# Optimization experiments

Hardware: AMD Instinct MI355X
Metric: run time of the kernel (lower is better)

Reference implementation:

```python
import jax, jax.numpy as jnp
import numpy as np

BINS = 256
EPS = 1e-8


def _norm255(x):
    # (x - min) / (max - min) * 255, truncated to int (torch .int())
    mx = jnp.max(x, axis=(2, 3), keepdims=True)
    mn = jnp.min(x, axis=(2, 3), keepdims=True)
    return ((x - mn) / (mx - mn) * 255.0).astype(jnp.int32)


def _hist256(x):
    # x int32 [B,C,H,W] -> per-(b,c) 256-bin histogram [B,C,256] float32
    B, C = x.shape[0], x.shape[1]
    flat = x.reshape(B * C, -1)
    rows = jnp.arange(B * C)[:, None]
    h = jnp.zeros((B * C, BINS), jnp.float32).at[rows, flat].add(1.0)
    return h.reshape(B, C, BINS)


def _entropy(x):
    # faithful to Entropy(): p = hist / (H*W); h = -sum p*log(p+1e-8)
    B, C, H, W = x.shape
    p = _hist256(x) / (H * W)
    h = -jnp.sum(p * jnp.log(p + EPS), axis=2)
    return h[:, :, None, None]  # [B,C,1,1]


def _joint_entropy(x_p, x_ms):
    # Faithful to Joint_entropy's quirky count: for each (i,j) it counts pixels
    # where (x_ms==i AND x_p==j) OR (x_ms!=i AND x_p!=j).
    # count[i,j] = 2*J[i,j] + npix - hist_ms[i] - hist_p[j], J = joint histogram.
    B, C, H, W = x_ms.shape
    npix = H * W
    bins = jnp.arange(BINS)
    M = (x_ms.reshape(B, C, npix)[..., None] == bins).astype(jnp.float32)  # [B,C,P,256]
    P = (x_p.reshape(B, npix)[..., None] == bins).astype(jnp.float32)      # [B,P,256]
    J = jnp.einsum('bcpi,bpj->bcij', M, P)                                  # [B,C,256,256]
    hist_ms = jnp.sum(M, axis=2)  # [B,C,256]
    hist_p = jnp.sum(P, axis=1)   # [B,256]
    count = 2.0 * J + npix - hist_ms[:, :, :, None] - hist_p[:, None, None, :]
    p = count / float(BINS * BINS)  # original divides by 256*256, not npix
    h = -jnp.sum(p * jnp.log(p + EPS), axis=(2, 3))
    return h[:, :, None, None]  # [B,C,1,1]


def _channel(f_p, f_ms):
    B, C, H, W = f_p.shape
    f_p_m = jnp.mean(f_p, axis=1, keepdims=True)  # [B,1,H,W]
    # AdaptiveAvgPool2d((16,16)) with H,W divisible by 16 == block mean
    pooled = f_p.reshape(B, C, 16, H // 16, 16, W // 16).mean(axis=(3, 5))
    f_p_a = jnp.mean(pooled, axis=1, keepdims=True)  # [B,1,16,16]
    f_ms_n = _norm255(f_ms)
    f_p_m_n = _norm255(f_p_m)
    f_p_a_n = _norm255(f_p_a)
    h_ms = _entropy(f_ms_n)                 # [B,C,1,1]
    h_p = _entropy(f_p_m_n)                 # [B,1,1,1]
    h_ms_p = _joint_entropy(f_p_a_n, f_ms_n)  # [B,C,1,1]
    mi = h_p + h_ms - h_ms_p
    mi = jax.nn.softmax(mi, axis=1)  # nn.Softmax() on 4D -> dim=1
    return f_ms + f_ms * mi


def _similarity(f_p, f_ms):
    B, C, H, W = f_p.shape
    f_ms_u = jax.image.resize(f_ms, (B, C, H, W), method='bilinear')
    a = f_ms_u.reshape(B, C, -1)
    b = f_p.reshape(B, C, -1)
    a = a - jnp.mean(a, axis=2, keepdims=True)
    b = b - jnp.mean(b, axis=2, keepdims=True)
    na = jnp.sqrt(jnp.sum(a * a, axis=2))  # [B,C] (ms norms)
    nb = jnp.sqrt(jnp.sum(b * b, axis=2))  # [B,C] (p norms)
    s = jnp.einsum('bcp,bdp->bcd', a, b)   # [B,C,C]
    return s / ((na * nb) / 100.0)[:, :, None]


def _spatial(f_p, f_ms):
    B, C, H, W = f_p.shape
    s_m = _similarity(f_p, f_ms)
    mx = jnp.max(s_m, axis=2)        # [B,C]
    idx = jnp.argmax(s_m, axis=2)    # [B,C] best f_p channel per ms channel
    scores = jax.nn.softmax(mx, axis=1)
    brow = jnp.arange(B)[:, None]
    # group score: sum of softmax scores of ms-channels that picked value v
    g = jnp.zeros((B, C), scores.dtype).at[brow, idx].add(scores)
    cnt = jnp.zeros((B, C), jnp.int32).at[brow, idx].add(1)
    k = jnp.min(jnp.sum(cnt > 0, axis=1))  # min #unique over batch
    min_k = (k + 1) // 2                   # ceil(min_k / 2)
    order = jnp.argsort(-g, axis=1)        # descending group score; absent groups (0) sort last
    sorted_scores = jnp.take_along_axis(g, order, axis=1)  # [B,C]
    pos_mask = jnp.arange(C) < min_k       # keep top min_k positions
    z = jnp.where(pos_mask[None, :], sorted_scores, -jnp.inf)
    w = jax.nn.softmax(z, axis=1)          # softmax over selected scores, 0 elsewhere
    gathered = jnp.take_along_axis(f_p, order[:, :, None, None], axis=1)  # [B,C,H,W]
    mask = jnp.sum(w[:, :, None, None] * jax.nn.sigmoid(gathered), axis=1, keepdims=True)
    return f_p + f_p * mask


def setup_inputs() -> dict:
    key = jax.random.key(0)
    k1, k2 = jax.random.split(key)
    f_p = jax.random.normal(k1, (8, 64, 256, 256), dtype=jnp.float32)
    f_ms = jax.random.normal(k2, (8, 64, 16, 16), dtype=jnp.float32)
    return {"f_p": f_p, "f_ms": f_ms}


def reference(f_p, f_ms):
    rel_ms = _channel(f_p, f_ms)
    rel_p = _spatial(f_p, f_ms)
    return (rel_p, rel_ms)
```

## Files before the change

kernel.cpp:

```cpp
#include <hip/hip_runtime.h>

#define BB 8
#define CC 64
#define HP 256
#define WP 256
#define PP 65536
#define QQ 256

__device__ __forceinline__ unsigned encF(float f) {
    unsigned u = __float_as_uint(f);
    return (u & 0x80000000u) ? ~u : (u | 0x80000000u);
}
__device__ __forceinline__ float decF(unsigned u) {
    unsigned b = (u & 0x80000000u) ? (u ^ 0x80000000u) : ~u;
    return __uint_as_float(b);
}

__device__ __forceinline__ double blockSumD(double v, double* red4) {
    int t = threadIdx.x;
    for (int d = 32; d; d >>= 1) v += __shfl_down(v, d, 64);
    __syncthreads();
    if ((t & 63) == 0) red4[t >> 6] = v;
    __syncthreads();
    double r = red4[0] + red4[1] + red4[2] + red4[3];
    __syncthreads();
    return r;
}

__global__ __launch_bounds__(256) void k34_fused(const float* __restrict__ fp,
                                                 const float* __restrict__ fms,
                                                 double* __restrict__ pasumD,
                                                 float* __restrict__ gtent,
                                                 double* __restrict__ chsumD,
                                                 double* __restrict__ chsumsqD,
                                                 int* __restrict__ msn,
                                                 int* __restrict__ histms,
                                                 float* __restrict__ hmsE,
                                                 float* __restrict__ naArr,
                                                 float* __restrict__ mssum) {
    int blk = blockIdx.x;
    if (blk < 4096) {
        int qg = blk & 7, c = (blk >> 3) & 63, b = blk >> 9;
        int x = threadIdx.x, s = x >> 4, r = x & 15;
        const float* src = fp + (size_t)(b * CC + c) * PP;
        __shared__ float tentL[256];
        __shared__ double red4[4];
        tentL[x] = 0.0f;
        __syncthreads();
        float wm, w0, wp;
        if (x <= 7)        { wm = 0.f; w0 = 1.f; wp = 0.f; }
        else if (x >= 248) { wm = 0.f; w0 = 1.f; wp = 0.f; }
        else if (r < 8)    { float fx = ((float)r + 8.5f) * 0.0625f; wm = 1.f - fx; w0 = fx;       wp = 0.f; }
        else               { float fx = ((float)r - 7.5f) * 0.0625f; wm = 0.f;      w0 = 1.f - fx; wp = fx;  }
        double sum = 0.0, ssq = 0.0;
#pragma unroll
        for (int qi = 0; qi < 2; ++qi) {
            int q = qg * 2 + qi;
            float am = 0.f, a0 = 0.f, ap = 0.f, cs = 0.f;
#pragma unroll
            for (int ry = 0; ry < 16; ++ry) {
                float v = src[(q * 16 + ry) * 256 + x];
                sum += (double)v;
                ssq += (double)v * (double)v;
                cs  += v;
                if ((q == 0 && ry < 8) || (q == 15 && ry >= 8)) {
                    a0 += v;
                } else if (ry < 8) {
                    float fy = ((float)ry + 8.5f) * 0.0625f;
                    am += (1.f - fy) * v; a0 += fy * v;
                } else {
                    float fy = ((float)ry - 7.5f) * 0.0625f;
                    a0 += (1.f - fy) * v; ap += fy * v;
                }
            }
            float vals[10];
            vals[0] = am * wm; vals[1] = am * w0; vals[2] = am * wp;
            vals[3] = a0 * wm; vals[4] = a0 * w0; vals[5] = a0 * wp;
            vals[6] = ap * wm; vals[7] = ap * w0; vals[8] = ap * wp;
            vals[9] = cs;
#pragma unroll
            for (int d = 8; d; d >>= 1) {
#pragma unroll
                for (int k2 = 0; k2 < 10; ++k2) vals[k2] += __shfl_down(vals[k2], d, 16);
            }
            if (r == 0) {
                if (q > 0) {
                    if (s > 0)  atomicAdd(&tentL[(q - 1) * 16 + (s - 1)], vals[0]);
                    atomicAdd(&tentL[(q - 1) * 16 + s], vals[1]);
                    if (s < 15) atomicAdd(&tentL[(q - 1) * 16 + (s + 1)], vals[2]);
                }
                if (s > 0)  atomicAdd(&tentL[q * 16 + (s - 1)], vals[3]);
                atomicAdd(&tentL[q * 16 + s], vals[4]);
                if (s < 15) atomicAdd(&tentL[q * 16 + (s + 1)], vals[5]);
                if (q < 15) {
                    if (s > 0)  atomicAdd(&tentL[(q + 1) * 16 + (s - 1)], vals[6]);
                    atomicAdd(&tentL[(q + 1) * 16 + s], vals[7]);
                    if (s < 15) atomicAdd(&tentL[(q + 1) * 16 + (s + 1)], vals[8]);
                }
                atomicAdd(&pasumD[b * 256 + q * 16 + s], (double)vals[9]);
            }
        }
        __syncthreads();
        int row = x >> 4;
        int rlo = qg * 2 - 1; if (rlo < 0) rlo = 0;
        int rhi = qg * 2 + 2; if (rhi > 15) rhi = 15;
        if (row >= rlo && row <= rhi) {
            atomicAdd(&gtent[(size_t)(b * CC + c) * QQ + x], tentL[x]);
        }
        double st = blockSumD(sum, red4);
        double sq = blockSumD(ssq, red4);
        if (x == 0) {
            atomicAdd(&chsumD[b * CC + c], st);
            atomicAdd(&chsumsqD[b * CC + c], sq);
        }
    } else {
        int blk2 = blk - 4096, b = blk2 >> 6, c = blk2 & 63, t = threadIdx.x;
        __shared__ float m[256];
        __shared__ int hist[256];
        __shared__ double red4[4];
        __shared__ double U[256];
        __shared__ unsigned umn, umx;
        float v = fms[(size_t)(b * CC + c) * QQ + t];
        m[t] = v;
        hist[t] = 0;
        if (t == 0) { umn = 0xFFFFFFFFu; umx = 0u; }
        float mn = v, mx = v;
        for (int d = 32; d; d >>= 1) {
            mn = fminf(mn, __shfl_down(mn, d, 64));
            mx = fmaxf(mx, __shfl_down(mx, d, 64));
        }
        __syncthreads();
        if ((t & 63) == 0) { atomicMin(&umn, encF(mn)); atomicMax(&umx, encF(mx)); }
        __syncthreads();
        mn = decF(umn); mx = decF(umx);
        int bin = (int)((v - mn) / (mx - mn) * 255.0f);
        bin = min(max(bin, 0), 255);
        msn[(size_t)(b * CC + c) * QQ + t] = bin;
        atomicAdd(&hist[bin], 1);
        __syncthreads();
        histms[(size_t)(b * CC + c) * QQ + t] = hist[t];
        float pf = (float)hist[t] * (1.0f / 256.0f);
        double term = -(double)(pf * __logf(pf + 1e-8f));
        double h = blockSumD(term, red4);
        if (t == 0) hmsE[b * CC + c] = (float)h;
        int i = t >> 4, j = t & 15;
        double kdj = (j == 0 || j == 15) ? 13.328125 : 10.65625;
        double mv = (double)m[t];
        double uu = kdj * mv + 2.671875 * ((j > 0 ? (double)m[t - 1] : 0.0) +
                                           (j < 15 ? (double)m[t + 1] : 0.0));
        U[t] = uu;
        __syncthreads();
        double kdi = (i == 0 || i == 15) ? 13.328125 : 10.65625;
        double vv = kdi * U[t] + 2.671875 * ((i > 0 ? U[t - 16] : 0.0) +
                                             (i < 15 ? U[t + 16] : 0.0));
        double sq = blockSumD(mv * vv, red4);
        double msm = blockSumD(mv, red4);
        if (t == 0) {
            mssum[b * CC + c] = (float)msm;
            double meanu = msm * (1.0 / 256.0);
            double na2 = sq - 65536.0 * meanu * meanu;
            naArr[b * CC + c] = (float)sqrt(na2 > 0.0 ? na2 : 0.0);
        }
    }
}

__global__ __launch_bounds__(256) void kC5_pa(const double* __restrict__ pasumD,
                                              int* __restrict__ pan,
                                              int* __restrict__ histp) {
    int b = blockIdx.x, t = threadIdx.x;
    __shared__ int hist[256];
    __shared__ unsigned umn, umx;
    hist[t] = 0;
    if (t == 0) { umn = 0xFFFFFFFFu; umx = 0u; }
    double acc = pasumD[b * 256 + t];
    float pa = (float)(acc * (1.0 / 256.0) * (1.0 / 64.0));
    float mn2 = pa, mx2 = pa;
    for (int d = 32; d; d >>= 1) {
        mn2 = fminf(mn2, __shfl_down(mn2, d, 64));
        mx2 = fmaxf(mx2, __shfl_down(mx2, d, 64));
    }
    __syncthreads();
    if ((t & 63) == 0) { atomicMin(&umn, encF(mn2)); atomicMax(&umx, encF(mx2)); }
    __syncthreads();
    mn2 = decF(umn); mx2 = decF(umx);
    int bin = (int)((pa - mn2) / (mx2 - mn2) * 255.0f);
    bin = min(max(bin, 0), 255);
    pan[b * QQ + t] = bin;
    atomicAdd(&hist[bin], 1);
    __syncthreads();
    histp[b * 256 + t] = hist[t];
}

__global__ __launch_bounds__(256) void k86_fused(const float* __restrict__ fms,
                                                 const float* __restrict__ gtent,
                                                 const float* __restrict__ mssum,
                                                 const double* __restrict__ chsumD,
                                                 const double* __restrict__ chsumsqD,
                                                 const float* __restrict__ naArr,
                                                 const int* __restrict__ msn,
                                                 const int* __restrict__ pan,
                                                 const int* __restrict__ histms,
                                                 const int* __restrict__ histp,
                                                 float* __restrict__ mxArr,
                                                 int* __restrict__ idxArr,
                                                 float* __restrict__ hjoint) {
    int blk0 = blockIdx.x;
    if (blk0 < 512) {
        int blk = blk0, b = blk >> 6, c = blk & 63, t = threadIdx.x;
        __shared__ float msrow[256];
        __shared__ double part[256];
        __shared__ double sval[64];
        msrow[t] = fms[(size_t)(b * CC + c) * QQ + t];
        __syncthreads();
        int d = t >> 2, pr = t & 3;
        const float* g = gtent + (size_t)(b * CC + d) * QQ + pr * 64;
        const float* mr = msrow + pr * 64;
        double acc = 0.0;
        for (int q2 = 0; q2 < 64; ++q2) acc += (double)mr[q2] * (double)g[q2];
        part[t] = acc;
        __syncthreads();
        if (t < 64) {
            double meanu = (double)mssum[b * CC + c] * (1.0 / 256.0);
            double meanp = chsumD[b * CC + t] * (1.0 / 65536.0);
            sval[t] = part[t * 4] + part[t * 4 + 1] + part[t * 4 + 2] + part[t * 4 + 3]
                      - 65536.0 * meanu * meanp;
        }
        __syncthreads();
        if (t == 0) {
            double best = sval[0]; int bi2 = 0;
            for (int dd = 1; dd < 64; ++dd) { if (sval[dd] > best) { best = sval[dd]; bi2 = dd; } }
            double nac = (double)naArr[b * CC + c];
            double sc_ = chsumD[b * CC + c];
            double sq_ = chsumsqD[b * CC + c];
            double nb2 = sq_ - sc_ * sc_ * (1.0 / 65536.0);
            double nbc = sqrt(nb2 > 0.0 ? nb2 : 0.0);
            mxArr[b * CC + c] = (float)(best * 100.0 / (nac * nbc));
            idxArr[b * CC + c] = bi2;
        }
    } else {
        int blk = blk0 - 512, b = blk >> 6, c = blk & 63, t = threadIdx.x;
        __shared__ int key[256], hms[256], hp[256];
        __shared__ double red4[4];
        int iv = msn[(size_t)(b * CC + c) * QQ + t];
        int jv = pan[b * QQ + t];
        key[t] = (iv << 8) | jv;
        hms[t] = histms[(size_t)(b * CC + c) * QQ + t];
        hp[t] = histp[b * 256 + t];
        __syncthreads();
        unsigned long long w0_ = 0, w1_ = 0, w2_ = 0, w3_ = 0;
        for (int p = 0; p < 256; ++p) {
            int k2 = key[p];
            if ((k2 >> 8) == t) {
                int j = k2 & 255;
                unsigned long long bit = 1ull << (j & 63);
                int w = j >> 6;
                if (w == 0) w0_ |= bit; else if (w == 1) w1_ |= bit;
                else if (w == 2) w2_ |= bit; else w3_ |= bit;
            }
        }
        double acc = 0.0;
        int basei = 256 - hms[t];
        unsigned long long words[4] = { w0_, w1_, w2_, w3_ };
#pragma unroll
        for (int w = 0; w < 4; ++w) {
            unsigned long long word = words[w];
            for (int jj = 0; jj < 64; ++jj) {
                if (!((word >> jj) & 1ull)) {
                    int cnt = basei - hp[w * 64 + jj];
                    float pf = (float)cnt * (1.0f / 65536.0f);
                    acc -= (double)(pf * __logf(pf + 1e-8f));
                }
            }
        }
        int myk = key[t], n = 0; bool first = true;
        for (int p = 0; p < 256; ++p) {
            int k2 = key[p];
            if (k2 == myk) { n++; if (p < t) first = false; }
        }
        if (first) {
            int cnt = 2 * n + 256 - hms[myk >> 8] - hp[myk & 255];
            float pf = (float)cnt * (1.0f / 65536.0f);
            acc -= (double)(pf * __logf(pf + 1e-8f));
        }
        double h = blockSumD(acc, red4);
        if (t == 0) hjoint[b * CC + c] = (float)h;
    }
}

__global__ __launch_bounds__(512) void k9_small(const float* __restrict__ mxArr,
                                                const int* __restrict__ idxArr,
                                                float* __restrict__ wsel,
                                                int* __restrict__ chanA,
                                                int* __restrict__ minkA) {
    __shared__ double sc[8][64];
    __shared__ double gs[8][64];
    __shared__ int idxS[8][64];
    __shared__ int ordv[8][64];
    __shared__ int uarr[8];
    __shared__ int mkS;
    int t = threadIdx.x;
    int b = t >> 6, c = t & 63;
    double v = (double)mxArr[b * 64 + c];
    double mx = v;
    for (int d = 32; d; d >>= 1) mx = fmax(mx, __shfl_down(mx, d, 64));
    mx = __shfl(mx, 0, 64);
    double e = exp(v - mx);
    double s = e;
    for (int d = 32; d; d >>= 1) s += __shfl_down(s, d, 64);
    s = __shfl(s, 0, 64);
    sc[b][c] = e / s;
    idxS[b][c] = idxArr[b * 64 + c];
    __syncthreads();
    double g = 0.0; int cnt = 0;
    for (int c2 = 0; c2 < 64; ++c2) {
        if (idxS[b][c2] == c) { g += sc[b][c2]; cnt++; }
    }
    gs[b][c] = g;
    unsigned long long ball = __ballot(cnt > 0);
    if (c == 0) uarr[b] = __popcll(ball);
    __syncthreads();
    if (t == 0) {
        int k = uarr[0];
        for (int b2 = 1; b2 < 8; ++b2) k = min(k, uarr[b2]);
        mkS = (k + 1) >> 1;
        minkA[0] = mkS;
    }
    __syncthreads();
    int rk = 0;
    double myg = gs[b][c];
    for (int c3 = 0; c3 < 64; ++c3) {
        double a = gs[b][c3];
        if (a > myg || (a == myg && c3 < c)) rk++;
    }
    ordv[b][rk] = c;
    __syncthreads();
    int mk = mkS;
    double z0 = gs[b][ordv[b][0]];
    double ee = (c < mk) ? exp(gs[b][ordv[b][c]] - z0) : 0.0;
    double se = ee;
    for (int d = 32; d; d >>= 1) se += __shfl_down(se, d, 64);
    se = __shfl(se, 0, 64);
    if (c < mk) {
        wsel[b * 64 + c] = (float)(ee / se);
        chanA[b * 64 + c] = ordv[b][c];
    }
}

__global__ __launch_bounds__(256) void k10_relp(const float* __restrict__ fp,
                                                const float* __restrict__ wsel,
                                                const int* __restrict__ chanA,
                                                const int* __restrict__ minkA,
                                                float* __restrict__ outp,
                                                float* __restrict__ fpm,
                                                unsigned* __restrict__ minmax) {
    int b = blockIdx.y;
    int i4 = blockIdx.x * 256 + threadIdx.x;
    int mk = minkA[0];
    const float4* src = (const float4*)(fp + (size_t)b * CC * PP);
    float mx0 = 0.f, mx1 = 0.f, mx2 = 0.f, mx3 = 0.f;
    for (int i = 0; i < mk; ++i) {
        int ch = chanA[b * 64 + i];
        float wv = wsel[b * 64 + i];
        float4 v = src[(size_t)ch * (PP / 4) + i4];
        mx0 += wv * (1.0f / (1.0f + __expf(-v.x)));
        mx1 += wv * (1.0f / (1.0f + __expf(-v.y)));
        mx2 += wv * (1.0f / (1.0f + __expf(-v.z)));
        mx3 += wv * (1.0f / (1.0f + __expf(-v.w)));
    }
    float sx = 0.f, sy = 0.f, sz = 0.f, sw = 0.f;
    float4* dst = (float4*)(outp + (size_t)b * CC * PP);
    for (int c2 = 0; c2 < CC; ++c2) {
        float4 v = src[(size_t)c2 * (PP / 4) + i4];
        sx += v.x; sy += v.y; sz += v.z; sw += v.w;
        float4 o;
        o.x = v.x + v.x * mx0;
        o.y = v.y + v.y * mx1;
        o.z = v.z + v.z * mx2;
        o.w = v.w + v.w * mx3;
        dst[(size_t)c2 * (PP / 4) + i4] = o;
    }
    const float inv = 1.0f / 64.0f;
    float4 m; m.x = sx * inv; m.y = sy * inv; m.z = sz * inv; m.w = sw * inv;
    ((float4*)(fpm + (size_t)b * PP))[i4] = m;
    float mn = fminf(fminf(m.x, m.y), fminf(m.z, m.w));
    float mxv = fmaxf(fmaxf(m.x, m.y), fmaxf(m.z, m.w));
    for (int d = 32; d; d >>= 1) {
        mn = fminf(mn, __shfl_down(mn, d, 64));
        mxv = fmaxf(mxv, __shfl_down(mxv, d, 64));
    }
    __shared__ unsigned smn, smx;
    if (threadIdx.x == 0) { smn = 0u; smx = 0u; }
    __syncthreads();
    if ((threadIdx.x & 63) == 0) { atomicMax(&smn, ~encF(mn)); atomicMax(&smx, encF(mxv)); }
    __syncthreads();
    if (threadIdx.x == 0) { atomicMax(&minmax[2 * b], smn); atomicMax(&minmax[2 * b + 1], smx); }
}

__global__ __launch_bounds__(256) void k2a_hist(const float* __restrict__ fpm,
                                                const unsigned* __restrict__ minmax,
                                                int* __restrict__ histpm) {
    int b = blockIdx.y;
    __shared__ int h[256];
    h[threadIdx.x] = 0;
    __syncthreads();
    float mn = decF(~minmax[2 * b]);
    float mx = decF(minmax[2 * b + 1]);
    float dd = mx - mn;
    int i4 = blockIdx.x * 256 + threadIdx.x;
    float4 v = ((const float4*)(fpm + (size_t)b * PP))[i4];
    int b0 = (int)((v.x - mn) / dd * 255.0f);
    int b1 = (int)((v.y - mn) / dd * 255.0f);
    int b2 = (int)((v.z - mn) / dd * 255.0f);
    int b3 = (int)((v.w - mn) / dd * 255.0f);
    b0 = min(max(b0, 0), 255); b1 = min(max(b1, 0), 255);
    b2 = min(max(b2, 0), 255); b3 = min(max(b3, 0), 255);
    atomicAdd(&h[b0], 1); atomicAdd(&h[b1], 1);
    atomicAdd(&h[b2], 1); atomicAdd(&h[b3], 1);
    __syncthreads();
    atomicAdd(&histpm[b * 256 + threadIdx.x], h[threadIdx.x]);
}

__global__ __launch_bounds__(256) void kF_relms(const int* __restrict__ histpm,
                                                const float* __restrict__ fms,
                                                const float* __restrict__ hmsE,
                                                const float* __restrict__ hjoint,
                                                float* __restrict__ out2) {
    int b = blockIdx.x, t = threadIdx.x;
    __shared__ double red4[4];
    __shared__ double mi[64];
    __shared__ float hpEs;
    int n = histpm[b * 256 + t];
    float p = (float)n * (1.0f / 65536.0f);
    double term = -(double)(p * __logf(p + 1e-8f));
    double h = blockSumD(term, red4);
    if (t == 0) hpEs = (float)h;
    __syncthreads();
    if (t < 64) mi[t] = (double)hpEs + (double)hmsE[b * CC + t] - (double)hjoint[b * CC + t];
    __syncthreads();
    if (t == 0) {
        double mxv = mi[0];
        for (int c2 = 1; c2 < 64; ++c2) if (mi[c2] > mxv) mxv = mi[c2];
        double s = 0.0;
        for (int c2 = 0; c2 < 64; ++c2) { mi[c2] = exp(mi[c2] - mxv); s += mi[c2]; }
        for (int c2 = 0; c2 < 64; ++c2) mi[c2] /= s;
    }
    __syncthreads();
    const float* srcm = fms + (size_t)b * CC * QQ;
    float* dstm = out2 + (size_t)b * CC * QQ;
    for (int e = t; e < CC * QQ; e += 256) {
        float v = srcm[e];
        float miv = (float)mi[e >> 8];
        dstm[e] = v + v * miv;
    }
}

extern "C" void kernel_launch(void* const* d_in, const int* in_sizes, int n_in,
                              void* d_out, int out_size, void* d_ws, size_t ws_size,
                              hipStream_t stream) {
    const float* fp = (const float*)d_in[0];
    const float* fms = (const float*)d_in[1];
    float* out = (float*)d_out;

    char* p = (char*)d_ws;
    auto alloc = [&](size_t bytes) { void* r = (void*)p; p += (bytes + 255) & ~(size_t)255; return r; };

    float* fpm      = (float*)alloc((size_t)BB * PP * 4);
    char* zbeg = p;
    float* gtent    = (float*)alloc((size_t)BB * CC * QQ * 4);
    double* pasumD  = (double*)alloc((size_t)BB * 256 * 8);
    double* chsumD  = (double*)alloc((size_t)BB * CC * 8);
    double* chsumsqD= (double*)alloc((size_t)BB * CC * 8);
    unsigned* minmax= (unsigned*)alloc((size_t)BB * 2 * 4);
    int* histpm     = (int*)alloc((size_t)BB * 256 * 4);
    size_t zlen = (size_t)(p - zbeg);
    int* msn        = (int*)alloc((size_t)BB * CC * QQ * 4);
    int* histms     = (int*)alloc((size_t)BB * CC * 256 * 4);
    int* histp      = (int*)alloc((size_t)BB * 256 * 4);
    int* pan        = (int*)alloc((size_t)BB * QQ * 4);
    float* hmsE     = (float*)alloc((size_t)BB * CC * 4);
    float* hjoint   = (float*)alloc((size_t)BB * CC * 4);
    float* naArr    = (float*)alloc((size_t)BB * CC * 4);
    float* mssum    = (float*)alloc((size_t)BB * CC * 4);
    float* mxArr    = (float*)alloc((size_t)BB * CC * 4);
    int* idxArr     = (int*)alloc((size_t)BB * CC * 4);
    float* wsel     = (float*)alloc((size_t)BB * CC * 4);
    int* chanA      = (int*)alloc((size_t)BB * CC * 4);
    int* minkA      = (int*)alloc(256);

    float* out_relp  = out;
    float* out_relms = out + (size_t)BB * CC * PP;

    hipMemsetAsync(zbeg, 0, zlen, stream);
    k34_fused<<<4608, 256, 0, stream>>>(fp, fms, pasumD, gtent, chsumD, chsumsqD,
                                        msn, histms, hmsE, naArr, mssum);
    kC5_pa<<<8, 256, 0, stream>>>(pasumD, pan, histp);
    k86_fused<<<1024, 256, 0, stream>>>(fms, gtent, mssum, chsumD, chsumsqD, naArr,
                                        msn, pan, histms, histp, mxArr, idxArr, hjoint);
    k9_small<<<1, 512, 0, stream>>>(mxArr, idxArr, wsel, chanA, minkA);
    k10_relp<<<dim3(64, 8), 256, 0, stream>>>(fp, wsel, chanA, minkA, out_relp, fpm, minmax);
    k2a_hist<<<dim3(64, 8), 256, 0, stream>>>(fpm, minmax, histpm);
    kF_relms<<<8, 256, 0, stream>>>(histpm, fms, hmsE, hjoint, out_relms);
}
```

Before: 383.8 us.

## Merge all stages into one persistent kernel with grid-wide barriers

Replaces the memset plus seven separate kernel launches with one persistent kernel of 1024 blocks. The stages are separated by a software grid barrier built on an atomic counter, and zeroing of the workspace moves inside the kernel. The goal is to remove launch gaps and tail idle time between the many small dependent stages. In exchange, phases that use only a few blocks (8 or 1) now leave the rest of the GPU waiting at spin barriers. Correctness also depends on all 1024 blocks being resident at the same time.

```diff
diff --git a/kernel.cpp b/kernel.cpp
--- a/kernel.cpp
+++ b/kernel.cpp
@@ -6,6 +6,8 @@
 #define WP 256
 #define PP 65536
 #define QQ 256
+#define NBLK 1024
+#define NTHR 256
 
 __device__ __forceinline__ unsigned encF(float f) {
     unsigned u = __float_as_uint(f);
@@ -27,430 +29,467 @@
     return r;
 }
 
-__global__ __launch_bounds__(256) void k34_fused(const float* __restrict__ fp,
-                                                 const float* __restrict__ fms,
-                                                 double* __restrict__ pasumD,
-                                                 float* __restrict__ gtent,
-                                                 double* __restrict__ chsumD,
-                                                 double* __restrict__ chsumsqD,
-                                                 int* __restrict__ msn,
-                                                 int* __restrict__ histms,
-                                                 float* __restrict__ hmsE,
-                                                 float* __restrict__ naArr,
-                                                 float* __restrict__ mssum) {
-    int blk = blockIdx.x;
-    if (blk < 4096) {
-        int qg = blk & 7, c = (blk >> 3) & 63, b = blk >> 9;
-        int x = threadIdx.x, s = x >> 4, r = x & 15;
-        const float* src = fp + (size_t)(b * CC + c) * PP;
-        __shared__ float tentL[256];
-        __shared__ double red4[4];
-        tentL[x] = 0.0f;
-        __syncthreads();
-        float wm, w0, wp;
-        if (x <= 7)        { wm = 0.f; w0 = 1.f; wp = 0.f; }
-        else if (x >= 248) { wm = 0.f; w0 = 1.f; wp = 0.f; }
-        else if (r < 8)    { float fx = ((float)r + 8.5f) * 0.0625f; wm = 1.f - fx; w0 = fx;       wp = 0.f; }
-        else               { float fx = ((float)r - 7.5f) * 0.0625f; wm = 0.f;      w0 = 1.f - fx; wp = fx;  }
-        double sum = 0.0, ssq = 0.0;
-#pragma unroll
-        for (int qi = 0; qi < 2; ++qi) {
-            int q = qg * 2 + qi;
-            float am = 0.f, a0 = 0.f, ap = 0.f, cs = 0.f;
-#pragma unroll
-            for (int ry = 0; ry < 16; ++ry) {
-                float v = src[(q * 16 + ry) * 256 + x];
-                sum += (double)v;
-                ssq += (double)v * (double)v;
-                cs  += v;
-                if ((q == 0 && ry < 8) || (q == 15 && ry >= 8)) {
-                    a0 += v;
-                } else if (ry < 8) {
-                    float fy = ((float)ry + 8.5f) * 0.0625f;
-                    am += (1.f - fy) * v; a0 += fy * v;
-                } else {
-                    float fy = ((float)ry - 7.5f) * 0.0625f;
-                    a0 += (1.f - fy) * v; ap += fy * v;
+__device__ __forceinline__ void gsync(unsigned* bar, unsigned phase) {
+    __syncthreads();
+    if (threadIdx.x == 0) {
+        __threadfence();
+        __hip_atomic_fetch_add(bar, 1u, __ATOMIC_RELEASE, __HIP_MEMORY_SCOPE_AGENT);
+        const unsigned target = phase * (unsigned)NBLK;
+        while (__hip_atomic_load(bar, __ATOMIC_ACQUIRE, __HIP_MEMORY_SCOPE_AGENT) < target) {
+            __builtin_amdgcn_s_sleep(4);
+        }
+        __threadfence();
+    }
+    __syncthreads();
+}
+
+__global__ __launch_bounds__(256, 4) void mega(
+        const float* __restrict__ fp, const float* __restrict__ fms,
+        float* __restrict__ outp, float* __restrict__ out2,
+        float* __restrict__ fpm, double* __restrict__ pasumD,
+        float* __restrict__ gtent, double* __restrict__ chsumD,
+        double* __restrict__ chsumsqD, unsigned* __restrict__ minmax,
+        int* __restrict__ histpm, int* __restrict__ msn,
+        int* __restrict__ histms, int* __restrict__ histp,
+        int* __restrict__ pan, float* __restrict__ hmsE,
+        float* __restrict__ hjoint, float* __restrict__ naArr,
+        float* __restrict__ mssum, float* __restrict__ mxArr,
+        int* __restrict__ idxArr, float* __restrict__ wsel,
+        int* __restrict__ chanA, int* __restrict__ minkA,
+        unsigned* __restrict__ barC) {
+    __shared__ __align__(16) char sm[12800];
+    const int blk = blockIdx.x;
+    const int tid = threadIdx.x;
+
+    {
+        int g = blk * NTHR + tid;
+        ((float2*)fpm)[g] = make_float2(0.f, 0.f);
+        if (g < BB * CC * QQ) gtent[g] = 0.f;
+        if (g < BB * 256) { pasumD[g] = 0.0; histpm[g] = 0; }
+        if (g < BB * CC) { chsumD[g] = 0.0; chsumsqD[g] = 0.0; }
+        if (g < BB * 2) minmax[g] = 0u;
+    }
+    gsync(barC, 1);
+
+    for (int vb = blk; vb < 4608; vb += NBLK) {
+        if (vb < 4096) {
+            int qg = vb & 7, c = (vb >> 3) & 63, b = vb >> 9;
+            int x = tid, s = x >> 4, r = x & 15;
+            const float* src = fp + (size_t)(b * CC + c) * PP;
+            float* tentL = (float*)sm;
+            double* red4 = (double*)(sm + 1024);
+            tentL[x] = 0.0f;
+            __syncthreads();
+            float wm, w0, wp;
+            if (x <= 7)        { wm = 0.f; w0 = 1.f; wp = 0.f; }
+            else if (x >= 248) { wm = 0.f; w0 = 1.f; wp = 0.f; }
+            else if (r < 8)    { float fx = ((float)r + 8.5f) * 0.0625f; wm = 1.f - fx; w0 = fx;       wp = 0.f; }
+            else               { float fx = ((float)r - 7.5f) * 0.0625f; wm = 0.f;      w0 = 1.f - fx; wp = fx;  }
+            double sum = 0.0, ssq = 0.0;
+#pragma unroll
+            for (int qi = 0; qi < 2; ++qi) {
+                int q = qg * 2 + qi;
+                float am = 0.f, a0 = 0.f, ap = 0.f, cs = 0.f;
+#pragma unroll
+                for (int ry = 0; ry < 16; ++ry) {
+                    float v = src[(q * 16 + ry) * 256 + x];
+                    sum += (double)v;
+                    ssq += (double)v * (double)v;
+                    cs  += v;
+                    if ((q == 0 && ry < 8) || (q == 15 && ry >= 8)) {
+                        a0 += v;
+                    } else if (ry < 8) {
+                        float fy = ((float)ry + 8.5f) * 0.0625f;
+                        am += (1.f - fy) * v; a0 += fy * v;
+                    } else {
+                        float fy = ((float)ry - 7.5f) * 0.0625f;
+                        a0 += (1.f - fy) * v; ap += fy * v;
+                    }
                 }
-            }
-            float vals[10];
-            vals[0] = am * wm; vals[1] = am * w0; vals[2] = am * wp;
-            vals[3] = a0 * wm; vals[4] = a0 * w0; vals[5] = a0 * wp;
-            vals[6] = ap * wm; vals[7] = ap * w0; vals[8] = ap * wp;
-            vals[9] = cs;
-#pragma unroll
-            for (int d = 8; d; d >>= 1) {
-#pragma unroll
-                for (int k2 = 0; k2 < 10; ++k2) vals[k2] += __shfl_down(vals[k2], d, 16);
-            }
-            if (r == 0) {
-                if (q > 0) {
-                    if (s > 0)  atomicAdd(&tentL[(q - 1) * 16 + (s - 1)], vals[0]);
-                    atomicAdd(&tentL[(q - 1) * 16 + s], vals[1]);
-                    if (s < 15) atomicAdd(&tentL[(q - 1) * 16 + (s + 1)], vals[2]);
+                float vals[10];
+                vals[0] = am * wm; vals[1] = am * w0; vals[2] = am * wp;
+                vals[3] = a0 * wm; vals[4] = a0 * w0; vals[5] = a0 * wp;
+                vals[6] = ap * wm; vals[7] = ap * w0; vals[8] = ap * wp;
+                vals[9] = cs;
+#pragma unroll
+                for (int d = 8; d; d >>= 1) {
+#pragma unroll
+                    for (int k2 = 0; k2 < 10; ++k2) vals[k2] += __shfl_down(vals[k2], d, 16);
                 }
-                if (s > 0)  atomicAdd(&tentL[q * 16 + (s - 1)], vals[3]);
-                atomicAdd(&tentL[q * 16 + s], vals[4]);
-                if (s < 15) atomicAdd(&tentL[q * 16 + (s + 1)], vals[5]);
-                if (q < 15) {
-                    if (s > 0)  atomicAdd(&tentL[(q + 1) * 16 + (s - 1)], vals[6]);
-                    atomicAdd(&tentL[(q + 1) * 16 + s], vals[7]);
-                    if (s < 15) atomicAdd(&tentL[(q + 1) * 16 + (s + 1)], vals[8]);
+                if (r == 0) {
+                    if (q > 0) {
+                        if (s > 0)  atomicAdd(&tentL[(q - 1) * 16 + (s - 1)], vals[0]);
+                        atomicAdd(&tentL[(q - 1) * 16 + s], vals[1]);
+                        if (s < 15) atomicAdd(&tentL[(q - 1) * 16 + (s + 1)], vals[2]);
+                    }
+                    if (s > 0)  atomicAdd(&tentL[q * 16 + (s - 1)], vals[3]);
+                    atomicAdd(&tentL[q * 16 + s], vals[4]);
+                    if (s < 15) atomicAdd(&tentL[q * 16 + (s + 1)], vals[5]);
+                    if (q < 15) {
+                        if (s > 0)  atomicAdd(&tentL[(q + 1) * 16 + (s - 1)], vals[6]);
+                        atomicAdd(&tentL[(q + 1) * 16 + s], vals[7]);
+                        if (s < 15) atomicAdd(&tentL[(q + 1) * 16 + (s + 1)], vals[8]);
+                    }
+                    atomicAdd(&pasumD[b * 256 + q * 16 + s], (double)vals[9]);
                 }
-                atomicAdd(&pasumD[b * 256 + q * 16 + s], (double)vals[9]);
-            }
-        }
-        __syncthreads();
-        int row = x >> 4;
-        int rlo = qg * 2 - 1; if (rlo < 0) rlo = 0;
-        int rhi = qg * 2 + 2; if (rhi > 15) rhi = 15;
-        if (row >= rlo && row <= rhi) {
-            atomicAdd(&gtent[(size_t)(b * CC + c) * QQ + x], tentL[x]);
-        }
-        double st = blockSumD(sum, red4);
-        double sq = blockSumD(ssq, red4);
-        if (x == 0) {
-            atomicAdd(&chsumD[b * CC + c], st);
-            atomicAdd(&chsumsqD[b * CC + c], sq);
-        }
-    } else {
-        int blk2 = blk - 4096, b = blk2 >> 6, c = blk2 & 63, t = threadIdx.x;
-        __shared__ float m[256];
-        __shared__ int hist[256];
-        __shared__ double red4[4];
-        __shared__ double U[256];
-        __shared__ unsigned umn, umx;
-        float v = fms[(size_t)(b * CC + c) * QQ + t];
-        m[t] = v;
+            }
+            __syncthreads();
+            int row = x >> 4;
+            int rlo = qg * 2 - 1; if (rlo < 0) rlo = 0;
+            int rhi = qg * 2 + 2; if (rhi > 15) rhi = 15;
+            if (row >= rlo && row <= rhi) {
+                atomicAdd(&gtent[(size_t)(b * CC + c) * QQ + x], tentL[x]);
+            }
+            double st = blockSumD(sum, red4);
+            double sq = blockSumD(ssq, red4);
+            if (x == 0) {
+                atomicAdd(&chsumD[b * CC + c], st);
+                atomicAdd(&chsumsqD[b * CC + c], sq);
+            }
+        } else {
+            int blk2 = vb - 4096, b = blk2 >> 6, c = blk2 & 63, t = tid;
+            float* m = (float*)sm;
+            int* hist = (int*)(sm + 1024);
+            double* U = (double*)(sm + 2048);
+            double* red4 = (double*)(sm + 4096);
+            unsigned* umn = (unsigned*)(sm + 4128);
+            unsigned* umx = (unsigned*)(sm + 4132);
+            float v = fms[(size_t)(b * CC + c) * QQ + t];
+            m[t] = v;
+            hist[t] = 0;
+            if (t == 0) { umn[0] = 0xFFFFFFFFu; umx[0] = 0u; }
+            float mn = v, mx = v;
+            for (int d = 32; d; d >>= 1) {
+                mn = fminf(mn, __shfl_down(mn, d, 64));
+                mx = fmaxf(mx, __shfl_down(mx, d, 64));
+            }
+            __syncthreads();
+            if ((t & 63) == 0) { atomicMin(umn, encF(mn)); atomicMax(umx, encF(mx)); }
+            __syncthreads();
+            mn = decF(umn[0]); mx = decF(umx[0]);
+            int bin = (int)((v - mn) / (mx - mn) * 255.0f);
+            bin = min(max(bin, 0), 255);
+            msn[(size_t)(b * CC + c) * QQ + t] = bin;
+            atomicAdd(&hist[bin], 1);
+            __syncthreads();
+            histms[(size_t)(b * CC + c) * QQ + t] = hist[t];
+            float pf = (float)hist[t] * (1.0f / 256.0f);
+            double term = -(double)(pf * __logf(pf + 1e-8f));
+            double h = blockSumD(term, red4);
+            if (t == 0) hmsE[b * CC + c] = (float)h;
+            int i = t >> 4, j = t & 15;
+            double kdj = (j == 0 || j == 15) ? 13.328125 : 10.65625;
+            double mv = (double)m[t];
+            double uu = kdj * mv + 2.671875 * ((j > 0 ? (double)m[t - 1] : 0.0) +
+                                               (j < 15 ? (double)m[t + 1] : 0.0));
+            U[t] = uu;
+            __syncthreads();
+            double kdi = (i == 0 || i == 15) ? 13.328125 : 10.65625;
+            double vv = kdi * U[t] + 2.671875 * ((i > 0 ? U[t - 16] : 0.0) +
+                                                 (i < 15 ? U[t + 16] : 0.0));
+            double sq = blockSumD(mv * vv, red4);
+            double msm = blockSumD(mv, red4);
+            if (t == 0) {
+                mssum[b * CC + c] = (float)msm;
+                double meanu = msm * (1.0 / 256.0);
+                double na2 = sq - 65536.0 * meanu * meanu;
+                naArr[b * CC + c] = (float)sqrt(na2 > 0.0 ? na2 : 0.0);
+            }
+        }
+    }
+    gsync(barC, 2);
+
+    if (blk < 8) {
+        int b = blk, t = tid;
+        int* hist = (int*)sm;
+        unsigned* umn = (unsigned*)(sm + 1024);
+        unsigned* umx = (unsigned*)(sm + 1028);
         hist[t] = 0;
-        if (t == 0) { umn = 0xFFFFFFFFu; umx = 0u; }
-        float mn = v, mx = v;
+        if (t == 0) { umn[0] = 0xFFFFFFFFu; umx[0] = 0u; }
+        double acc = pasumD[b * 256 + t];
+        float pa = (float)(acc * (1.0 / 256.0) * (1.0 / 64.0));
+        float mn2 = pa, mx2 = pa;
+        for (int d = 32; d; d >>= 1) {
+            mn2 = fminf(mn2, __shfl_down(mn2, d, 64));
+            mx2 = fmaxf(mx2, __shfl_down(mx2, d, 64));
+        }
+        __syncthreads();
+        if ((t & 63) == 0) { atomicMin(umn, encF(mn2)); atomicMax(umx, encF(mx2)); }
+        __syncthreads();
+        mn2 = decF(umn[0]); mx2 = decF(umx[0]);
+        int bin = (int)((pa - mn2) / (mx2 - mn2) * 255.0f);
+        bin = min(max(bin, 0), 255);
+        pan[b * QQ + t] = bin;
+        atomicAdd(&hist[bin], 1);
+        __syncthreads();
+        histp[b * 256 + t] = hist[t];
+    }
+    gsync(barC, 3);
+
+    {
+        if (blk < 512) {
+            int b = blk >> 6, c = blk & 63, t = tid;
+            float* msrow = (float*)sm;
+            double* part = (double*)(sm + 1024);
+            double* sval = (double*)(sm + 3072);
+            msrow[t] = fms[(size_t)(b * CC + c) * QQ + t];
+            __syncthreads();
+            int d = t >> 2, pr = t & 3;
+            const float* g = gtent + (size_t)(b * CC + d) * QQ + pr * 64;
+            const float* mr = msrow + pr * 64;
+            double acc = 0.0;
+            for (int q2 = 0; q2 < 64; ++q2) acc += (double)mr[q2] * (double)g[q2];
+            part[t] = acc;
+            __syncthreads();
+            if (t < 64) {
+                double meanu = (double)mssum[b * CC + c] * (1.0 / 256.0);
+                double meanp = chsumD[b * CC + t] * (1.0 / 65536.0);
+                sval[t] = part[t * 4] + part[t * 4 + 1] + part[t * 4 + 2] + part[t * 4 + 3]
+                          - 65536.0 * meanu * meanp;
+            }
+            __syncthreads();
+            if (t == 0) {
+                double best = sval[0]; int bi2 = 0;
+                for (int dd = 1; dd < 64; ++dd) { if (sval[dd] > best) { best = sval[dd]; bi2 = dd; } }
+                double nac = (double)naArr[b * CC + c];
+                double sc_ = chsumD[b * CC + c];
+                double sq_ = chsumsqD[b * CC + c];
+                double nb2 = sq_ - sc_ * sc_ * (1.0 / 65536.0);
+                double nbc = sqrt(nb2 > 0.0 ? nb2 : 0.0);
+                mxArr[b * CC + c] = (float)(best * 100.0 / (nac * nbc));
+                idxArr[b * CC + c] = bi2;
+            }
+        } else {
+            int vb = blk - 512, b = vb >> 6, c = vb & 63, t = tid;
+            int* key = (int*)sm;
+            int* hms = (int*)(sm + 1024);
+            int* hp = (int*)(sm + 2048);
+            double* red4 = (double*)(sm + 3072);
+            int iv = msn[(size_t)(b * CC + c) * QQ + t];
+            int jv = pan[b * QQ + t];
+            key[t] = (iv << 8) | jv;
+            hms[t] = histms[(size_t)(b * CC + c) * QQ + t];
+            hp[t] = histp[b * 256 + t];
+            __syncthreads();
+            unsigned long long w0_ = 0, w1_ = 0, w2_ = 0, w3_ = 0;
+            for (int p = 0; p < 256; ++p) {
+                int k2 = key[p];
+                if ((k2 >> 8) == t) {
+                    int j = k2 & 255;
+                    unsigned long long bit = 1ull << (j & 63);
+                    int w = j >> 6;
+                    if (w == 0) w0_ |= bit; else if (w == 1) w1_ |= bit;
+                    else if (w == 2) w2_ |= bit; else w3_ |= bit;
+                }
+            }
+            double acc = 0.0;
+            int basei = 256 - hms[t];
+            unsigned long long words[4] = { w0_, w1_, w2_, w3_ };
+#pragma unroll
+            for (int w = 0; w < 4; ++w) {
+                unsigned long long word = words[w];
+                for (int jj = 0; jj < 64; ++jj) {
+                    if (!((word >> jj) & 1ull)) {
+                        int cnt = basei - hp[w * 64 + jj];
+                        float pf = (float)cnt * (1.0f / 65536.0f);
+                        acc -= (double)(pf * __logf(pf + 1e-8f));
+                    }
+                }
+            }
+            int myk = key[t], n = 0; bool first = true;
+            for (int p = 0; p < 256; ++p) {
+                int k2 = key[p];
+                if (k2 == myk) { n++; if (p < t) first = false; }
+            }
+            if (first) {
+                int cnt = 2 * n + 256 - hms[myk >> 8] - hp[myk & 255];
+                float pf = (float)cnt * (1.0f / 65536.0f);
+                acc -= (double)(pf * __logf(pf + 1e-8f));
+            }
+            double h = blockSumD(acc, red4);
+            if (t == 0) hjoint[b * CC + c] = (float)h;
+        }
+    }
+    gsync(barC, 4);
+
+    if (blk == 0) {
+        double* sc = (double*)sm;
+        double* gs = (double*)(sm + 4096);
+        int* idxS = (int*)(sm + 8192);
+        int* ordv = (int*)(sm + 10240);
+        int* uarr = (int*)(sm + 12288);
+        int* mkS  = (int*)(sm + 12320);
+        int t = tid, c = t & 63, wv = t >> 6;
+#pragma unroll
+        for (int pass = 0; pass < 2; ++pass) {
+            int b = wv + pass * 4;
+            double v = (double)mxArr[b * 64 + c];
+            double mx = v;
+            for (int d = 32; d; d >>= 1) mx = fmax(mx, __shfl_down(mx, d, 64));
+            mx = __shfl(mx, 0, 64);
+            double e = exp(v - mx);
+            double s = e;
+            for (int d = 32; d; d >>= 1) s += __shfl_down(s, d, 64);
+            s = __shfl(s, 0, 64);
+            sc[b * 64 + c] = e / s;
+            idxS[b * 64 + c] = idxArr[b * 64 + c];
+        }
+        __syncthreads();
+#pragma unroll
+        for (int pass = 0; pass < 2; ++pass) {
+            int b = wv + pass * 4;
+            double g = 0.0; int cnt = 0;
+            for (int c2 = 0; c2 < 64; ++c2) {
+                if (idxS[b * 64 + c2] == c) { g += sc[b * 64 + c2]; cnt++; }
+            }
+            gs[b * 64 + c] = g;
+            unsigned long long ball = __ballot(cnt > 0);
+            if (c == 0) uarr[b] = __popcll(ball);
+        }
+        __syncthreads();
+        if (t == 0) {
+            int k = uarr[0];
+            for (int b2 = 1; b2 < 8; ++b2) k = min(k, uarr[b2]);
+            mkS[0] = (k + 1) >> 1;
+            minkA[0] = mkS[0];
+        }
+        __syncthreads();
+#pragma unroll
+        for (int pass = 0; pass < 2; ++pass) {
+            int b = wv + pass * 4;
+            int rk = 0;
+            double myg = gs[b * 64 + c];
+            for (int c3 = 0; c3 < 64; ++c3) {
+                double a = gs[b * 64 + c3];
+                if (a > myg || (a == myg && c3 < c)) rk++;
+            }
+            ordv[b * 64 + rk] = c;
+        }
+        __syncthreads();
+#pragma unroll
+        for (int pass = 0; pass < 2; ++pass) {
+            int b = wv + pass * 4;
+            int mk = mkS[0];
+            double z0 = gs[b * 64 + ordv[b * 64 + 0]];
+            double ee = (c < mk) ? exp(gs[b * 64 + ordv[b * 64 + c]] - z0) : 0.0;
+            double se = ee;
+            for (int d = 32; d; d >>= 1) se += __shfl_down(se, d, 64);
+            se = __shfl(se, 0, 64);
+            if (c < mk) {
+                wsel[b * 64 + c] = (float)(ee / se);
+                chanA[b * 64 + c] = ordv[b * 64 + c];
+            }
+        }
+    }
+    gsync(barC, 5);
+
+    {
+        int half = blk >> 9;
+        int b = (blk >> 6) & 7;
+        int ih = blk & 63;
+        int i4 = ih * 256 + tid;
+        int mk = minkA[0];
+        const float4* src = (const float4*)(fp + (size_t)b * CC * PP);
+        float mx0 = 0.f, mx1 = 0.f, mx2 = 0.f, mx3 = 0.f;
+        for (int i = 0; i < mk; ++i) {
+            int ch = chanA[b * 64 + i];
+            float wv = wsel[b * 64 + i];
+            float4 v = src[(size_t)ch * (PP / 4) + i4];
+            mx0 += wv * (1.0f / (1.0f + __expf(-v.x)));
+            mx1 += wv * (1.0f / (1.0f + __expf(-v.y)));
+            mx2 += wv * (1.0f / (1.0f + __expf(-v.z)));
+            mx3 += wv * (1.0f / (1.0f + __expf(-v.w)));
+        }
+        float sx = 0.f, sy = 0.f, sz = 0.f, sw = 0.f;
+        float4* dst = (float4*)(outp + (size_t)b * CC * PP);
+        int c0 = half * 32;
+        for (int c2 = c0; c2 < c0 + 32; ++c2) {
+            float4 v = src[(size_t)c2 * (PP / 4) + i4];
+            sx += v.x; sy += v.y; sz += v.z; sw += v.w;
+            float4 o;
+            o.x = v.x + v.x * mx0;
+            o.y = v.y + v.y * mx1;
+            o.z = v.z + v.z * mx2;
+            o.w = v.w + v.w * mx3;
+            dst[(size_t)c2 * (PP / 4) + i4] = o;
+        }
+        float* fb = fpm + (size_t)b * PP + (size_t)i4 * 4;
+        atomicAdd(&fb[0], sx); atomicAdd(&fb[1], sy);
+        atomicAdd(&fb[2], sz); atomicAdd(&fb[3], sw);
+    }
+    gsync(barC, 6);
+
+    if (blk < 512) {
+        int b = blk >> 6;
+        int i4 = (blk & 63) * 256 + tid;
+        unsigned* smn = (unsigned*)sm;
+        unsigned* smx = (unsigned*)(sm + 4);
+        float4 m = ((const float4*)(fpm + (size_t)b * PP))[i4];
+        float mn = fminf(fminf(m.x, m.y), fminf(m.z, m.w));
+        float mxv = fmaxf(fmaxf(m.x, m.y), fmaxf(m.z, m.w));
         for (int d = 32; d; d >>= 1) {
             mn = fminf(mn, __shfl_down(mn, d, 64));
-            mx = fmaxf(mx, __shfl_down(mx, d, 64));
-        }
-        __syncthreads();
-        if ((t & 63) == 0) { atomicMin(&umn, encF(mn)); atomicMax(&umx, encF(mx)); }
-        __syncthreads();
-        mn = decF(umn); mx = decF(umx);
-        int bin = (int)((v - mn) / (mx - mn) * 255.0f);
-        bin = min(max(bin, 0), 255);
-        msn[(size_t)(b * CC + c) * QQ + t] = bin;
-        atomicAdd(&hist[bin], 1);
-        __syncthreads();
-        histms[(size_t)(b * CC + c) * QQ + t] = hist[t];
-        float pf = (float)hist[t] * (1.0f / 256.0f);
-        double term = -(double)(pf * __logf(pf + 1e-8f));
+            mxv = fmaxf(mxv, __shfl_down(mxv, d, 64));
+        }
+        if (tid == 0) { smn[0] = 0u; smx[0] = 0u; }
+        __syncthreads();
+        if ((tid & 63) == 0) { atomicMax(smn, ~encF(mn)); atomicMax(smx, encF(mxv)); }
+        __syncthreads();
+        if (tid == 0) { atomicMax(&minmax[2 * b], smn[0]); atomicMax(&minmax[2 * b + 1], smx[0]); }
+    }
+    gsync(barC, 7);
+
+    if (blk < 512) {
+        int b = blk >> 6;
+        int* h = (int*)sm;
+        h[tid] = 0;
+        __syncthreads();
+        float mn = decF(~minmax[2 * b]);
+        float mx = decF(minmax[2 * b + 1]);
+        float dd = mx - mn;
+        int i4 = (blk & 63) * 256 + tid;
+        float4 v = ((const float4*)(fpm + (size_t)b * PP))[i4];
+        int b0 = (int)((v.x - mn) / dd * 255.0f);
+        int b1 = (int)((v.y - mn) / dd * 255.0f);
+        int b2 = (int)((v.z - mn) / dd * 255.0f);
+        int b3 = (int)((v.w - mn) / dd * 255.0f);
+        b0 = min(max(b0, 0), 255); b1 = min(max(b1, 0), 255);
+        b2 = min(max(b2, 0), 255); b3 = min(max(b3, 0), 255);
+        atomicAdd(&h[b0], 1); atomicAdd(&h[b1], 1);
+        atomicAdd(&h[b2], 1); atomicAdd(&h[b3], 1);
+        __syncthreads();
+        atomicAdd(&histpm[b * 256 + tid], h[tid]);
+    }
+    gsync(barC, 8);
+
+    if (blk < 8) {
+        int b = blk, t = tid;
+        double* red4 = (double*)sm;
+        double* mi = (double*)(sm + 32);
+        float* hpEs = (float*)(sm + 544);
+        int n = histpm[b * 256 + t];
+        float p = (float)n * (1.0f / 65536.0f);
+        double term = -(double)(p * __logf(p + 1e-8f));
         double h = blockSumD(term, red4);
-        if (t == 0) hmsE[b * CC + c] = (float)h;
-        int i = t >> 4, j = t & 15;
-        double kdj = (j == 0 || j == 15) ? 13.328125 : 10.65625;
-        double mv = (double)m[t];
-        double uu = kdj * mv + 2.671875 * ((j > 0 ? (double)m[t - 1] : 0.0) +
-                                           (j < 15 ? (double)m[t + 1] : 0.0));
-        U[t] = uu;
-        __syncthreads();
-        double kdi = (i == 0 || i == 15) ? 13.328125 : 10.65625;
-        double vv = kdi * U[t] + 2.671875 * ((i > 0 ? U[t - 16] : 0.0) +
-                                             (i < 15 ? U[t + 16] : 0.0));
-        double sq = blockSumD(mv * vv, red4);
-        double msm = blockSumD(mv, red4);
+        if (t == 0) hpEs[0] = (float)h;
+        __syncthreads();
+        if (t < 64) mi[t] = (double)hpEs[0] + (double)hmsE[b * CC + t] - (double)hjoint[b * CC + t];
+        __syncthreads();
         if (t == 0) {
-            mssum[b * CC + c] = (float)msm;
-            double meanu = msm * (1.0 / 256.0);
-            double na2 = sq - 65536.0 * meanu * meanu;
-            naArr[b * CC + c] = (float)sqrt(na2 > 0.0 ? na2 : 0.0);
-        }
-    }
-}
-
-__global__ __launch_bounds__(256) void kC5_pa(const double* __restrict__ pasumD,
-                                              int* __restrict__ pan,
-                                              int* __restrict__ histp) {
-    int b = blockIdx.x, t = threadIdx.x;
-    __shared__ int hist[256];
-    __shared__ unsigned umn, umx;
-    hist[t] = 0;
-    if (t == 0) { umn = 0xFFFFFFFFu; umx = 0u; }
-    double acc = pasumD[b * 256 + t];
-    float pa = (float)(acc * (1.0 / 256.0) * (1.0 / 64.0));
-    float mn2 = pa, mx2 = pa;
-    for (int d = 32; d; d >>= 1) {
-        mn2 = fminf(mn2, __shfl_down(mn2, d, 64));
-        mx2 = fmaxf(mx2, __shfl_down(mx2, d, 64));
-    }
-    __syncthreads();
-    if ((t & 63) == 0) { atomicMin(&umn, encF(mn2)); atomicMax(&umx, encF(mx2)); }
-    __syncthreads();
-    mn2 = decF(umn); mx2 = decF(umx);
-    int bin = (int)((pa - mn2) / (mx2 - mn2) * 255.0f);
-    bin = min(max(bin, 0), 255);
-    pan[b * QQ + t] = bin;
-    atomicAdd(&hist[bin], 1);
-    __syncthreads();
-    histp[b * 256 + t] = hist[t];
-}
-
-__global__ __launch_bounds__(256) void k86_fused(const float* __restrict__ fms,
-                                                 const float* __restrict__ gtent,
-                                                 const float* __restrict__ mssum,
-                                                 const double* __restrict__ chsumD,
-                                                 const double* __restrict__ chsumsqD,
-                                                 const float* __restrict__ naArr,
-                                                 const int* __restrict__ msn,
-                                                 const int* __restrict__ pan,
-                                                 const int* __restrict__ histms,
-                                                 const int* __restrict__ histp,
-                                                 float* __restrict__ mxArr,
-                                                 int* __restrict__ idxArr,
-                                                 float* __restrict__ hjoint) {
-    int blk0 = blockIdx.x;
-    if (blk0 < 512) {
-        int blk = blk0, b = blk >> 6, c = blk & 63, t = threadIdx.x;
-        __shared__ float msrow[256];
-        __shared__ double part[256];
-        __shared__ double sval[64];
-        msrow[t] = fms[(size_t)(b * CC + c) * QQ + t];
-        __syncthreads();
-        int d = t >> 2, pr = t & 3;
-        const float* g = gtent + (size_t)(b * CC + d) * QQ + pr * 64;
-        const float* mr = msrow + pr * 64;
-        double acc = 0.0;
-        for (int q2 = 0; q2 < 64; ++q2) acc += (double)mr[q2] * (double)g[q2];
-        part[t] = acc;
-        __syncthreads();
-        if (t < 64) {
-            double meanu = (double)mssum[b * CC + c] * (1.0 / 256.0);
-            double meanp = chsumD[b * CC + t] * (1.0 / 65536.0);
-            sval[t] = part[t * 4] + part[t * 4 + 1] + part[t * 4 + 2] + part[t * 4 + 3]
-                      - 65536.0 * meanu * meanp;
-        }
-        __syncthreads();
-        if (t == 0) {
-            double best = sval[0]; int bi2 = 0;
-            for (int dd = 1; dd < 64; ++dd) { if (sval[dd] > best) { best = sval[dd]; bi2 = dd; } }
-            double nac = (double)naArr[b * CC + c];
-            double sc_ = chsumD[b * CC + c];
-            double sq_ = chsumsqD[b * CC + c];
-            double nb2 = sq_ - sc_ * sc_ * (1.0 / 65536.0);
-            double nbc = sqrt(nb2 > 0.0 ? nb2 : 0.0);
-            mxArr[b * CC + c] = (float)(best * 100.0 / (nac * nbc));
-            idxArr[b * CC + c] = bi2;
-        }
-    } else {
-        int blk = blk0 - 512, b = blk >> 6, c = blk & 63, t = threadIdx.x;
-        __shared__ int key[256], hms[256], hp[256];
-        __shared__ double red4[4];
-        int iv = msn[(size_t)(b * CC + c) * QQ + t];
-        int jv = pan[b * QQ + t];
-        key[t] = (iv << 8) | jv;
-        hms[t] = histms[(size_t)(b * CC + c) * QQ + t];
-        hp[t] = histp[b * 256 + t];
-        __syncthreads();
-        unsigned long long w0_ = 0, w1_ = 0, w2_ = 0, w3_ = 0;
-        for (int p = 0; p < 256; ++p) {
-            int k2 = key[p];
-            if ((k2 >> 8) == t) {
-                int j = k2 & 255;
-                unsigned long long bit = 1ull << (j & 63);
-                int w = j >> 6;
-                if (w == 0) w0_ |= bit; else if (w == 1) w1_ |= bit;
-                else if (w == 2) w2_ |= bit; else w3_ |= bit;
-            }
-        }
-        double acc = 0.0;
-        int basei = 256 - hms[t];
-        unsigned long long words[4] = { w0_, w1_, w2_, w3_ };
-#pragma unroll
-        for (int w = 0; w < 4; ++w) {
-            unsigned long long word = words[w];
-            for (int jj = 0; jj < 64; ++jj) {
-                if (!((word >> jj) & 1ull)) {
-                    int cnt = basei - hp[w * 64 + jj];
-                    float pf = (float)cnt * (1.0f / 65536.0f);
-                    acc -= (double)(pf * __logf(pf + 1e-8f));
-                }
-            }
-        }
-        int myk = key[t], n = 0; bool first = true;
-        for (int p = 0; p < 256; ++p) {
-            int k2 = key[p];
-            if (k2 == myk) { n++; if (p < t) first = false; }
-        }
-        if (first) {
-            int cnt = 2 * n + 256 - hms[myk >> 8] - hp[myk & 255];
-            float pf = (float)cnt * (1.0f / 65536.0f);
-            acc -= (double)(pf * __logf(pf + 1e-8f));
-        }
-        double h = blockSumD(acc, red4);
-        if (t == 0) hjoint[b * CC + c] = (float)h;
-    }
-}
-
-__global__ __launch_bounds__(512) void k9_small(const float* __restrict__ mxArr,
-                                                const int* __restrict__ idxArr,
-                                                float* __restrict__ wsel,
-                                                int* __restrict__ chanA,
-                                                int* __restrict__ minkA) {
-    __shared__ double sc[8][64];
-    __shared__ double gs[8][64];
-    __shared__ int idxS[8][64];
-    __shared__ int ordv[8][64];
-    __shared__ int uarr[8];
-    __shared__ int mkS;
-    int t = threadIdx.x;
-    int b = t >> 6, c = t & 63;
-    double v = (double)mxArr[b * 64 + c];
-    double mx = v;
-    for (int d = 32; d; d >>= 1) mx = fmax(mx, __shfl_down(mx, d, 64));
-    mx = __shfl(mx, 0, 64);
-    double e = exp(v - mx);
-    double s = e;
-    for (int d = 32; d; d >>= 1) s += __shfl_down(s, d, 64);
-    s = __shfl(s, 0, 64);
-    sc[b][c] = e / s;
-    idxS[b][c] = idxArr[b * 64 + c];
-    __syncthreads();
-    double g = 0.0; int cnt = 0;
-    for (int c2 = 0; c2 < 64; ++c2) {
-        if (idxS[b][c2] == c) { g += sc[b][c2]; cnt++; }
-    }
-    gs[b][c] = g;
-    unsigned long long ball = __ballot(cnt > 0);
-    if (c == 0) uarr[b] = __popcll(ball);
-    __syncthreads();
-    if (t == 0) {
-        int k = uarr[0];
-        for (int b2 = 1; b2 < 8; ++b2) k = min(k, uarr[b2]);
-        mkS = (k + 1) >> 1;
-        minkA[0] = mkS;
-    }
-    __syncthreads();
-    int rk = 0;
-    double myg = gs[b][c];
-    for (int c3 = 0; c3 < 64; ++c3) {
-        double a = gs[b][c3];
-        if (a > myg || (a == myg && c3 < c)) rk++;
-    }
-    ordv[b][rk] = c;
-    __syncthreads();
-    int mk = mkS;
-    double z0 = gs[b][ordv[b][0]];
-    double ee = (c < mk) ? exp(gs[b][ordv[b][c]] - z0) : 0.0;
-    double se = ee;
-    for (int d = 32; d; d >>= 1) se += __shfl_down(se, d, 64);
-    se = __shfl(se, 0, 64);
-    if (c < mk) {
-        wsel[b * 64 + c] = (float)(ee / se);
-        chanA[b * 64 + c] = ordv[b][c];
-    }
-}
-
-__global__ __launch_bounds__(256) void k10_relp(const float* __restrict__ fp,
-                                                const float* __restrict__ wsel,
-                                                const int* __restrict__ chanA,
-                                                const int* __restrict__ minkA,
-                                                float* __restrict__ outp,
-                                                float* __restrict__ fpm,
-                                                unsigned* __restrict__ minmax) {
-    int b = blockIdx.y;
-    int i4 = blockIdx.x * 256 + threadIdx.x;
-    int mk = minkA[0];
-    const float4* src = (const float4*)(fp + (size_t)b * CC * PP);
-    float mx0 = 0.f, mx1 = 0.f, mx2 = 0.f, mx3 = 0.f;
-    for (int i = 0; i < mk; ++i) {
-        int ch = chanA[b * 64 + i];
-        float wv = wsel[b * 64 + i];
-        float4 v = src[(size_t)ch * (PP / 4) + i4];
-        mx0 += wv * (1.0f / (1.0f + __expf(-v.x)));
-        mx1 += wv * (1.0f / (1.0f + __expf(-v.y)));
-        mx2 += wv * (1.0f / (1.0f + __expf(-v.z)));
-        mx3 += wv * (1.0f / (1.0f + __expf(-v.w)));
-    }
-    float sx = 0.f, sy = 0.f, sz = 0.f, sw = 0.f;
-    float4* dst = (float4*)(outp + (size_t)b * CC * PP);
-    for (int c2 = 0; c2 < CC; ++c2) {
-        float4 v = src[(size_t)c2 * (PP / 4) + i4];
-        sx += v.x; sy += v.y; sz += v.z; sw += v.w;
-        float4 o;
-        o.x = v.x + v.x * mx0;
-        o.y = v.y + v.y * mx1;
-        o.z = v.z + v.z * mx2;
-        o.w = v.w + v.w * mx3;
-        dst[(size_t)c2 * (PP / 4) + i4] = o;
-    }
-    const float inv = 1.0f / 64.0f;
-    float4 m; m.x = sx * inv; m.y = sy * inv; m.z = sz * inv; m.w = sw * inv;
-    ((float4*)(fpm + (size_t)b * PP))[i4] = m;
-    float mn = fminf(fminf(m.x, m.y), fminf(m.z, m.w));
-    float mxv = fmaxf(fmaxf(m.x, m.y), fmaxf(m.z, m.w));
-    for (int d = 32; d; d >>= 1) {
-        mn = fminf(mn, __shfl_down(mn, d, 64));
-        mxv = fmaxf(mxv, __shfl_down(mxv, d, 64));
-    }
-    __shared__ unsigned smn, smx;
-    if (threadIdx.x == 0) { smn = 0u; smx = 0u; }
-    __syncthreads();
-    if ((threadIdx.x & 63) == 0) { atomicMax(&smn, ~encF(mn)); atomicMax(&smx, encF(mxv)); }
-    __syncthreads();
-    if (threadIdx.x == 0) { atomicMax(&minmax[2 * b], smn); atomicMax(&minmax[2 * b + 1], smx); }
-}
-
-__global__ __launch_bounds__(256) void k2a_hist(const float* __restrict__ fpm,
-                                                const unsigned* __restrict__ minmax,
-                                                int* __restrict__ histpm) {
-    int b = blockIdx.y;
-    __shared__ int h[256];
-    h[threadIdx.x] = 0;
-    __syncthreads();
-    float mn = decF(~minmax[2 * b]);
-    float mx = decF(minmax[2 * b + 1]);
-    float dd = mx - mn;
-    int i4 = blockIdx.x * 256 + threadIdx.x;
-    float4 v = ((const float4*)(fpm + (size_t)b * PP))[i4];
-    int b0 = (int)((v.x - mn) / dd * 255.0f);
-    int b1 = (int)((v.y - mn) / dd * 255.0f);
-    int b2 = (int)((v.z - mn) / dd * 255.0f);
-    int b3 = (int)((v.w - mn) / dd * 255.0f);
-    b0 = min(max(b0, 0), 255); b1 = min(max(b1, 0), 255);
-    b2 = min(max(b2, 0), 255); b3 = min(max(b3, 0), 255);
-    atomicAdd(&h[b0], 1); atomicAdd(&h[b1], 1);
-    atomicAdd(&h[b2], 1); atomicAdd(&h[b3], 1);
-    __syncthreads();
-    atomicAdd(&histpm[b * 256 + threadIdx.x], h[threadIdx.x]);
-}
-
-__global__ __launch_bounds__(256) void kF_relms(const int* __restrict__ histpm,
-                                                const float* __restrict__ fms,
-                                                const float* __restrict__ hmsE,
-                                                const float* __restrict__ hjoint,
-                                                float* __restrict__ out2) {
-    int b = blockIdx.x, t = threadIdx.x;
-    __shared__ double red4[4];
-    __shared__ double mi[64];
-    __shared__ float hpEs;
-    int n = histpm[b * 256 + t];
-    float p = (float)n * (1.0f / 65536.0f);
-    double term = -(double)(p * __logf(p + 1e-8f));
-    double h = blockSumD(term, red4);
-    if (t == 0) hpEs = (float)h;
-    __syncthreads();
-    if (t < 64) mi[t] = (double)hpEs + (double)hmsE[b * CC + t] - (double)hjoint[b * CC + t];
-    __syncthreads();
-    if (t == 0) {
-        double mxv = mi[0];
-        for (int c2 = 1; c2 < 64; ++c2) if (mi[c2] > mxv) mxv = mi[c2];
-        double s = 0.0;
-        for (int c2 = 0; c2 < 64; ++c2) { mi[c2] = exp(mi[c2] - mxv); s += mi[c2]; }
-        for (int c2 = 0; c2 < 64; ++c2) mi[c2] /= s;
-    }
-    __syncthreads();
-    const float* srcm = fms + (size_t)b * CC * QQ;
-    float* dstm = out2 + (size_t)b * CC * QQ;
-    for (int e = t; e < CC * QQ; e += 256) {
-        float v = srcm[e];
-        float miv = (float)mi[e >> 8];
-        dstm[e] = v + v * miv;
+            double mxv = mi[0];
+            for (int c2 = 1; c2 < 64; ++c2) if (mi[c2] > mxv) mxv = mi[c2];
+            double s = 0.0;
+            for (int c2 = 0; c2 < 64; ++c2) { mi[c2] = exp(mi[c2] - mxv); s += mi[c2]; }
+            for (int c2 = 0; c2 < 64; ++c2) mi[c2] /= s;
+        }
+        __syncthreads();
+        const float* srcm = fms + (size_t)b * CC * QQ;
+        float* dstm = out2 + (size_t)b * CC * QQ;
+        for (int e = t; e < CC * QQ; e += 256) {
+            float v = srcm[e];
+            float miv = (float)mi[e >> 8];
+            dstm[e] = v + v * miv;
+        }
     }
 }
 
@@ -465,14 +504,12 @@
     auto alloc = [&](size_t bytes) { void* r = (void*)p; p += (bytes + 255) & ~(size_t)255; return r; };
 
     float* fpm      = (float*)alloc((size_t)BB * PP * 4);
-    char* zbeg = p;
     float* gtent    = (float*)alloc((size_t)BB * CC * QQ * 4);
     double* pasumD  = (double*)alloc((size_t)BB * 256 * 8);
     double* chsumD  = (double*)alloc((size_t)BB * CC * 8);
     double* chsumsqD= (double*)alloc((size_t)BB * CC * 8);
     unsigned* minmax= (unsigned*)alloc((size_t)BB * 2 * 4);
     int* histpm     = (int*)alloc((size_t)BB * 256 * 4);
-    size_t zlen = (size_t)(p - zbeg);
     int* msn        = (int*)alloc((size_t)BB * CC * QQ * 4);
     int* histms     = (int*)alloc((size_t)BB * CC * 256 * 4);
     int* histp      = (int*)alloc((size_t)BB * 256 * 4);
@@ -486,18 +523,15 @@
     float* wsel     = (float*)alloc((size_t)BB * CC * 4);
     int* chanA      = (int*)alloc((size_t)BB * CC * 4);
     int* minkA      = (int*)alloc(256);
+    unsigned* barC  = (unsigned*)alloc(256);
 
     float* out_relp  = out;
     float* out_relms = out + (size_t)BB * CC * PP;
 
-    hipMemsetAsync(zbeg, 0, zlen, stream);
-    k34_fused<<<4608, 256, 0, stream>>>(fp, fms, pasumD, gtent, chsumD, chsumsqD,
-                                        msn, histms, hmsE, naArr, mssum);
-    kC5_pa<<<8, 256, 0, stream>>>(pasumD, pan, histp);
-    k86_fused<<<1024, 256, 0, stream>>>(fms, gtent, mssum, chsumD, chsumsqD, naArr,
-                                        msn, pan, histms, histp, mxArr, idxArr, hjoint);
-    k9_small<<<1, 512, 0, stream>>>(mxArr, idxArr, wsel, chanA, minkA);
-    k10_relp<<<dim3(64, 8), 256, 0, stream>>>(fp, wsel, chanA, minkA, out_relp, fpm, minmax);
-    k2a_hist<<<dim3(64, 8), 256, 0, stream>>>(fpm, minmax, histpm);
-    kF_relms<<<8, 256, 0, stream>>>(histpm, fms, hmsE, hjoint, out_relms);
+    hipMemsetAsync(barC, 0, 256, stream);
+    mega<<<NBLK, NTHR, 0, stream>>>(fp, fms, out_relp, out_relms,
+                                    fpm, pasumD, gtent, chsumD, chsumsqD,
+                                    minmax, histpm, msn, histms, histp, pan,
+                                    hmsE, hjoint, naArr, mssum, mxArr, idxArr,
+                                    wsel, chanA, minkA, barC);
 }
```

New measurement: 1.329 ms. 3.46x slower.
